# Performance work log

Measured on AMD Instinct MI355X. Metric: run time of the kernel, lower is better.

The kernel has to match this reference:

```python
import jax, jax.numpy as jnp
import numpy as np

T, N, E = 8, 5000, 160000
IN_DIM, HID, H = 64, 128, 8
D = HID // H  # head dim = 16
NC = 2
EPS = 1e-5


def layer_norm(x, g, b):
    mu = jnp.mean(x, axis=-1, keepdims=True)
    var = jnp.mean((x - mu) ** 2, axis=-1, keepdims=True)
    return (x - mu) / jnp.sqrt(var + EPS) * g + b


def setup_inputs() -> dict:
    key = jax.random.key(0)
    ks = jax.random.split(key, 24)
    p = {}
    p["x"] = jax.random.normal(ks[0], (T, N, IN_DIM), dtype=jnp.float32)
    p["edge_index"] = jax.random.randint(ks[1], (T, 2, E), 0, N, dtype=jnp.int32)
    p["noise"] = jax.random.normal(ks[2], (N, HID), dtype=jnp.float32)
    def w(k, shape, fan_in):
        return jax.random.normal(k, shape, dtype=jnp.float32) * (1.0 / np.sqrt(fan_in))
    p["W_proj"] = w(ks[3], (IN_DIM, HID), IN_DIM)
    p["b_proj"] = jnp.zeros((HID,), jnp.float32)
    p["W_gat"] = w(ks[4], (HID, HID), HID)
    p["a_src"] = w(ks[5], (H, D), D)
    p["a_dst"] = w(ks[6], (H, D), D)
    p["b_gat"] = jnp.zeros((HID,), jnp.float32)
    p["g1"] = jnp.ones((HID,), jnp.float32)
    p["be1"] = jnp.zeros((HID,), jnp.float32)
    p["W_qkv"] = w(ks[7], (3 * HID, HID), HID)
    p["b_qkv"] = jnp.zeros((3 * HID,), jnp.float32)
    p["W_o"] = w(ks[8], (HID, HID), HID)
    p["b_o"] = jnp.zeros((HID,), jnp.float32)
    p["g2"] = jnp.ones((HID,), jnp.float32)
    p["be2"] = jnp.zeros((HID,), jnp.float32)
    p["Wc1"] = w(ks[9], (HID, HID), HID)
    p["bc1"] = jnp.zeros((HID,), jnp.float32)
    p["gc"] = jnp.ones((HID,), jnp.float32)
    p["bec"] = jnp.zeros((HID,), jnp.float32)
    p["Wc2"] = w(ks[10], (HID, NC), HID)
    p["bc2"] = jnp.array([0.0, 0.1], jnp.float32)
    return p


def reference(x, edge_index, noise, W_proj, b_proj, W_gat, a_src, a_dst, b_gat,
              g1, be1, W_qkv, b_qkv, W_o, b_o, g2, be2,
              Wc1, bc1, gc, bec, Wc2, bc2):
    # per-timestep projection + ReLU: [T, N, HID]
    h = jax.nn.relu(x @ W_proj + b_proj)

    loop = jnp.arange(N, dtype=edge_index.dtype)

    def gat(h_t, ei):  # h_t: [N, HID], ei: [2, E]
        src = jnp.concatenate([ei[0], loop])  # add self loops
        dst = jnp.concatenate([ei[1], loop])
        xh = (h_t @ W_gat).reshape(N, H, D)          # [N, H, D]
        a_s = jnp.sum(xh * a_src, axis=-1)           # [N, H]
        a_d = jnp.sum(xh * a_dst, axis=-1)           # [N, H]
        e = jax.nn.leaky_relu(a_s[src] + a_d[dst], 0.2)  # [E', H]
        m = jax.ops.segment_max(e, dst, num_segments=N)
        ex = jnp.exp(e - m[dst])
        s = jax.ops.segment_sum(ex, dst, num_segments=N)
        alpha = ex / (s[dst] + 1e-16)                # segment softmax per dst/head
        out = jax.ops.segment_sum(xh[src] * alpha[..., None], dst, num_segments=N)
        return out.reshape(N, HID) + b_gat

    feats = jax.vmap(gat)(h, edge_index)             # [T, N, HID]
    nf = jnp.transpose(feats, (1, 0, 2))             # [N, T, HID] (node = batch)

    nrm = layer_norm(nf, g1, be1)
    qkv = nrm @ W_qkv.T + b_qkv                      # [N, T, 3*HID]
    q, k, v = jnp.split(qkv, 3, axis=-1)
    def heads(t):
        return t.reshape(N, T, H, D).transpose(0, 2, 1, 3)  # [N, H, T, D]
    q, k, v = heads(q), heads(k), heads(v)
    scores = jnp.einsum('nhqd,nhkd->nhqk', q, k) / jnp.sqrt(jnp.float32(D))
    attn = jax.nn.softmax(scores, axis=-1)
    ta = jnp.einsum('nhqk,nhkd->nhqd', attn, v)
    ta = ta.transpose(0, 2, 1, 3).reshape(N, T, HID) @ W_o.T + b_o

    fused = layer_norm(nf + ta, g2, be2)
    emb = fused[:, -1, :]                            # [N, HID]

    node_ids = jnp.arange(N, dtype=jnp.float32) / N
    div = jnp.sin(node_ids * 6.28) * 0.1             # [N]
    emb = emb + div[:, None] + noise * 0.05          # eval noise scale

    h1 = emb @ Wc1 + bc1
    h1 = jax.nn.gelu(layer_norm(h1, gc, bec), approximate=False)
    logits = h1 @ Wc2 + bc2                          # [N, 2]
    sinu = jnp.sin(jnp.arange(N, dtype=jnp.float32) * 0.5) * 0.2
    logits = logits.at[:, 1].add(sinu)
    return emb, logits
```

## Files before the change

### kernel.cpp

```cpp
#include <hip/hip_runtime.h>
#include <math.h>

#define T 8
#define N 5000
#define E 160000
#define EN (E + N)
#define IN_DIM 64
#define HID 128
#define H 8
#define D 16
#define NC 2
#define MT 32
#define NB 4

__device__ __forceinline__ float leaky(float e) { return (e >= 0.0f) ? e : 0.2f * e; }

__global__ __launch_bounds__(256) void k_pg(const float* __restrict__ x,
                                            const float* __restrict__ Wp,
                                            const float* __restrict__ bp,
                                            const float* __restrict__ Wg,
                                            const float* __restrict__ asrc,
                                            const float* __restrict__ adst,
                                            float* __restrict__ xh,
                                            float* __restrict__ a_s,
                                            float* __restrict__ a_d,
                                            int* __restrict__ cursor) {
    __shared__ float xt[MT][IN_DIM];
    __shared__ float ht[MT][HID + 1];
    int row0 = blockIdx.x * MT;
    int tid = threadIdx.x;

    {
        int gi = blockIdx.x * 256 + tid;
        if (gi < T * N) cursor[gi] = 0;
    }

    for (int idx = tid; idx < MT * IN_DIM; idx += 256) {
        int r = idx >> 6, k = idx & 63;
        xt[r][k] = x[(size_t)(row0 + r) * IN_DIM + k];
    }
    __syncthreads();

    int cg = tid & 31;
    int rg = tid >> 5;
    int c0 = cg * 4, r0 = rg * 4;

    {
        float4 b4 = *(const float4*)(bp + c0);
        float a00=b4.x,a01=b4.y,a02=b4.z,a03=b4.w;
        float a10=b4.x,a11=b4.y,a12=b4.z,a13=b4.w;
        float a20=b4.x,a21=b4.y,a22=b4.z,a23=b4.w;
        float a30=b4.x,a31=b4.y,a32=b4.z,a33=b4.w;
        for (int k = 0; k < IN_DIM; ++k) {
            float4 w = *(const float4*)(Wp + (size_t)k * HID + c0);
            float x0 = xt[r0 + 0][k], x1 = xt[r0 + 1][k];
            float x2 = xt[r0 + 2][k], x3 = xt[r0 + 3][k];
            a00 += x0*w.x; a01 += x0*w.y; a02 += x0*w.z; a03 += x0*w.w;
            a10 += x1*w.x; a11 += x1*w.y; a12 += x1*w.z; a13 += x1*w.w;
            a20 += x2*w.x; a21 += x2*w.y; a22 += x2*w.z; a23 += x2*w.w;
            a30 += x3*w.x; a31 += x3*w.y; a32 += x3*w.z; a33 += x3*w.w;
        }
        ht[r0+0][c0+0]=fmaxf(a00,0.f); ht[r0+0][c0+1]=fmaxf(a01,0.f);
        ht[r0+0][c0+2]=fmaxf(a02,0.f); ht[r0+0][c0+3]=fmaxf(a03,0.f);
        ht[r0+1][c0+0]=fmaxf(a10,0.f); ht[r0+1][c0+1]=fmaxf(a11,0.f);
        ht[r0+1][c0+2]=fmaxf(a12,0.f); ht[r0+1][c0+3]=fmaxf(a13,0.f);
        ht[r0+2][c0+0]=fmaxf(a20,0.f); ht[r0+2][c0+1]=fmaxf(a21,0.f);
        ht[r0+2][c0+2]=fmaxf(a22,0.f); ht[r0+2][c0+3]=fmaxf(a23,0.f);
        ht[r0+3][c0+0]=fmaxf(a30,0.f); ht[r0+3][c0+1]=fmaxf(a31,0.f);
        ht[r0+3][c0+2]=fmaxf(a32,0.f); ht[r0+3][c0+3]=fmaxf(a33,0.f);
    }
    __syncthreads();

    float a00=0,a01=0,a02=0,a03=0, a10=0,a11=0,a12=0,a13=0;
    float a20=0,a21=0,a22=0,a23=0, a30=0,a31=0,a32=0,a33=0;
    for (int k = 0; k < HID; ++k) {
        float4 w = *(const float4*)(Wg + (size_t)k * HID + c0);
        float h0 = ht[r0 + 0][k], h1 = ht[r0 + 1][k];
        float h2 = ht[r0 + 2][k], h3 = ht[r0 + 3][k];
        a00 += h0*w.x; a01 += h0*w.y; a02 += h0*w.z; a03 += h0*w.w;
        a10 += h1*w.x; a11 += h1*w.y; a12 += h1*w.z; a13 += h1*w.w;
        a20 += h2*w.x; a21 += h2*w.y; a22 += h2*w.z; a23 += h2*w.w;
        a30 += h3*w.x; a31 += h3*w.y; a32 += h3*w.z; a33 += h3*w.w;
    }
    {
        float4 v;
        v.x=a00; v.y=a01; v.z=a02; v.w=a03;
        *(float4*)(xh + (size_t)(row0 + r0 + 0) * HID + c0) = v;
        v.x=a10; v.y=a11; v.z=a12; v.w=a13;
        *(float4*)(xh + (size_t)(row0 + r0 + 1) * HID + c0) = v;
        v.x=a20; v.y=a21; v.z=a22; v.w=a23;
        *(float4*)(xh + (size_t)(row0 + r0 + 2) * HID + c0) = v;
        v.x=a30; v.y=a31; v.z=a32; v.w=a33;
        *(float4*)(xh + (size_t)(row0 + r0 + 3) * HID + c0) = v;
    }
    __syncthreads();
    ht[r0+0][c0+0]=a00; ht[r0+0][c0+1]=a01; ht[r0+0][c0+2]=a02; ht[r0+0][c0+3]=a03;
    ht[r0+1][c0+0]=a10; ht[r0+1][c0+1]=a11; ht[r0+1][c0+2]=a12; ht[r0+1][c0+3]=a13;
    ht[r0+2][c0+0]=a20; ht[r0+2][c0+1]=a21; ht[r0+2][c0+2]=a22; ht[r0+2][c0+3]=a23;
    ht[r0+3][c0+0]=a30; ht[r0+3][c0+1]=a31; ht[r0+3][c0+2]=a32; ht[r0+3][c0+3]=a33;
    __syncthreads();

    {
        int r = tid >> 3, hh = tid & 7;
        float s1 = 0.0f, s2 = 0.0f;
        #pragma unroll
        for (int d = 0; d < D; ++d) {
            float v = ht[r][hh * D + d];
            s1 += v * asrc[hh * D + d];
            s2 += v * adst[hh * D + d];
        }
        a_s[(size_t)(row0 + r) * H + hh] = s1;
        a_d[(size_t)(row0 + r) * H + hh] = s2;
    }
}

__global__ void k_tr(const float* __restrict__ W_qkv, const float* __restrict__ W_o,
                     float* __restrict__ WTq, float* __restrict__ WoT) {
    int idx = blockIdx.x * 256 + threadIdx.x;
    if (idx < 384 * 128) {
        int j = idx >> 7, c = idx & 127;
        WTq[c * 384 + j] = W_qkv[idx];
    } else if (idx < 384 * 128 + 128 * 128) {
        int r = idx - 384 * 128;
        int j = r >> 7, k = r & 127;
        WoT[k * 128 + j] = W_o[r];
    }
}

__global__ __launch_bounds__(256) void k_hist(const int* __restrict__ ei,
                                              int* __restrict__ cursor) {
    __shared__ int hist[N];
    int t = blockIdx.x >> 3;
    int chunk = blockIdx.x & 7;
    int tid = threadIdx.x;

    for (int i = tid; i < N; i += 256) hist[i] = 0;
    __syncthreads();

    const int CS = (EN + 7) / 8;
    int i0 = chunk * CS;
    int i1 = (i0 + CS < EN) ? i0 + CS : EN;
    const int* drow = ei + (size_t)(2 * t + 1) * E;
    for (int i = i0 + tid; i < i1; i += 256) {
        int d = (i < E) ? drow[i] : (i - E);
        atomicAdd(&hist[d], 1);
    }
    __syncthreads();

    int* cur = cursor + t * N;
    for (int i = tid; i < N; i += 256) {
        int c = hist[i];
        if (c) atomicAdd(&cur[i], c);
    }
}

__global__ void k_scan(int* __restrict__ cursor, int* __restrict__ offs) {
    __shared__ int part[256];
    int t = blockIdx.x;
    int tid = threadIdx.x;
    const int CH = 20;
    int begin = tid * CH;
    int sum = 0;
    for (int k = 0; k < CH; ++k) {
        int i = begin + k;
        if (i < N) sum += cursor[t * N + i];
    }
    part[tid] = sum;
    __syncthreads();
    if (tid == 0) {
        int run = 0;
        for (int i = 0; i < 256; ++i) { int v = part[i]; part[i] = run; run += v; }
        offs[t * (N + 1) + N] = run;
    }
    __syncthreads();
    int run = part[tid];
    for (int k = 0; k < CH; ++k) {
        int i = begin + k;
        if (i < N) {
            int cnt = cursor[t * N + i];
            offs[t * (N + 1) + i] = run;
            cursor[t * N + i] = run;
            run += cnt;
        }
    }
}

__global__ __launch_bounds__(256) void k_scatter(const int* __restrict__ ei,
                                                 int* __restrict__ cursor,
                                                 int* __restrict__ csr_src) {
    const int PT = EN / 4;
    int idx = blockIdx.x * 256 + threadIdx.x;
    int t = idx / PT;
    if (t >= T) return;
    int e0 = idx - t * PT;

    const int* srow = ei + (size_t)(2 * t) * E;
    const int* drow = srow + E;
    int s[4], d[4];
    #pragma unroll
    for (int j = 0; j < 4; ++j) {
        int i = e0 + j * PT;
        if (i < E) { s[j] = srow[i]; d[j] = drow[i]; }
        else       { s[j] = d[j] = i - E; }
    }
    int* cur = cursor + t * N;
    int p[4];
    #pragma unroll
    for (int j = 0; j < 4; ++j) p[j] = atomicAdd(&cur[d[j]], 1);
    int* csb = csr_src + (size_t)t * EN;
    #pragma unroll
    for (int j = 0; j < 4; ++j) csb[p[j]] = s[j];
}

__global__ __launch_bounds__(128) void k_aggc(
        const int* __restrict__ offs, const int* __restrict__ csr_src,
        const float* __restrict__ a_s, const float* __restrict__ a_d,
        const float* __restrict__ xh, const float* __restrict__ b_gat,
        const float* __restrict__ g1, const float* __restrict__ be1,
        float* __restrict__ nrm, float* __restrict__ xlast_g) {
    int b = blockIdx.x;
    int t = b & 7;
    int dst = b >> 3;
    int tid = threadIdx.x;

    int o0 = offs[t * (N + 1) + dst];
    int o1 = offs[t * (N + 1) + dst + 1];
    int deg = o1 - o0;
    const int* esrc = csr_src + (size_t)t * EN + o0;
    const float* as_b = a_s + (size_t)t * N * H;
    const float* ad_b = a_d + (size_t)t * N * H;
    const float* xh_b = xh + (size_t)t * N * HID;

    __shared__ float lal[16][H];
    __shared__ int   lsrc[16];
    __shared__ float ws_s[2][H];
    __shared__ float pacc[2][HID];
    __shared__ float red[128];

    int eh_e = tid >> 3, eh_h = tid & 7;
    int el = tid >> 5, cg = tid & 31;
    int hg = cg >> 2;
    float adh_e = ad_b[dst * H + eh_h];

    float4 acc = {0.0f, 0.0f, 0.0f, 0.0f};
    float wpart = 0.0f;

    int ntile = (deg + 15) >> 4;
    for (int tt = 0; tt < ntile; ++tt) {
        int ej = (tt << 4) + eh_e;
        float w = 0.0f;
        int src = 0;
        if (ej < deg) {
            src = esrc[ej];
            w = expf(leaky(as_b[src * H + eh_h] + adh_e));
        }
        if (eh_h == 0) lsrc[eh_e] = src;
        lal[eh_e][eh_h] = w;
        wpart += w;
        __syncthreads();
        #pragma unroll
        for (int jj = 0; jj < 4; ++jj) {
            int j = (jj << 2) + el;
            int s = lsrc[j];
            float l = lal[j][hg];
            float4 v = *(const float4*)(xh_b + (size_t)s * HID + (cg << 2));
            acc.x += l * v.x; acc.y += l * v.y;
            acc.z += l * v.z; acc.w += l * v.w;
        }
        __syncthreads();
    }

    {
        float w = wpart;
        w += __shfl_xor(w, 8);
        w += __shfl_xor(w, 16);
        w += __shfl_xor(w, 32);
        if ((tid & 63) < 8) ws_s[tid >> 6][eh_h] = w;
    }
    acc.x += __shfl_xor(acc.x, 32);
    acc.y += __shfl_xor(acc.y, 32);
    acc.z += __shfl_xor(acc.z, 32);
    acc.w += __shfl_xor(acc.w, 32);
    if (!(tid & 32)) *(float4*)&pacc[tid >> 6][(tid & 31) << 2] = acc;
    __syncthreads();

    int hh = tid >> 4;
    float wsum = ws_s[0][hh] + ws_s[1][hh];
    float val = (pacc[0][tid] + pacc[1][tid]) / (wsum + 1e-16f);

    float v = val + b_gat[tid];
    red[tid] = v;
    __syncthreads();
    if (tid < 64) {
        float s = red[tid] + red[tid + 64];
        #pragma unroll
        for (int m = 1; m < 64; m <<= 1) s += __shfl_xor(s, m);
        if (tid == 0) red[0] = s;
    }
    __syncthreads();
    float mu = red[0] * (1.0f / HID);
    __syncthreads();
    float dv = v - mu;
    red[tid] = dv * dv;
    __syncthreads();
    if (tid < 64) {
        float s = red[tid] + red[tid + 64];
        #pragma unroll
        for (int m = 1; m < 64; m <<= 1) s += __shfl_xor(s, m);
        if (tid == 0) red[0] = s;
    }
    __syncthreads();
    float rstd = rsqrtf(red[0] * (1.0f / HID) + 1e-5f);

    nrm[(size_t)(dst * T + t) * HID + tid] = dv * rstd * g1[tid] + be1[tid];
    if (t == T - 1) xlast_g[(size_t)dst * HID + tid] = v;
}

__global__ __launch_bounds__(256) void k_fuse(
        const float* __restrict__ nrm,
        const float* __restrict__ WTq,
        const float* __restrict__ b_qkv,
        const float* __restrict__ xlast_g,
        const float* __restrict__ WoT,
        const float* __restrict__ b_o,
        const float* __restrict__ g2, const float* __restrict__ be2,
        const float* __restrict__ noise, float* __restrict__ out) {
    __shared__ float at[NB * T][HID];
    __shared__ float ql[NB][HID];
    __shared__ float ws[8][384];
    float* ta_s = &at[0][0];

    int n0 = blockIdx.x * NB;
    int tid = threadIdx.x;
    int cg = tid & 31, rg = tid >> 5;
    int c0 = cg * 4, r0 = rg * 4;
    int u = rg >> 1;

    {
        const float* srcp = nrm + (size_t)n0 * T * HID;
        for (int idx = tid; idx < NB * T * 32; idx += 256) {
            int r = idx >> 5, c4 = (idx & 31) << 2;
            *(float4*)&at[r][c4] = *(const float4*)(srcp + (size_t)r * HID + c4);
        }
    }

    float ka[4][4], va[4][4], qa[4];
    {
        float4 bk = *(const float4*)(b_qkv + 128 + c0);
        float4 bv = *(const float4*)(b_qkv + 256 + c0);
        #pragma unroll
        for (int i = 0; i < 4; ++i) {
            ka[i][0] = bk.x; ka[i][1] = bk.y; ka[i][2] = bk.z; ka[i][3] = bk.w;
            va[i][0] = bv.x; va[i][1] = bv.y; va[i][2] = bv.z; va[i][3] = bv.w;
        }
        if (rg < 4) {
            float4 bq = *(const float4*)(b_qkv + c0);
            qa[0] = bq.x; qa[1] = bq.y; qa[2] = bq.z; qa[3] = bq.w;
        } else {
            qa[0] = qa[1] = qa[2] = qa[3] = 0.0f;
        }
    }
    __syncthreads();

    const float* atq = at[(rg & 3) * T + (T - 1)];

    for (int kc = 0; kc < 16; ++kc) {
        #pragma unroll
        for (int j = 0; j < 3; ++j) {
            int f = j * 256 + tid;
            int row = f / 96;
            int cc = (f - row * 96) << 2;
            *(float4*)&ws[row][cc] =
                *(const float4*)(WTq + (size_t)(kc * 8 + row) * 384 + cc);
        }
        __syncthreads();

        #pragma unroll
        for (int kk = 0; kk < 8; kk += 4) {
            int k = kc * 8 + kk;
            float4 e0 = *(const float4*)&at[r0 + 0][k];
            float4 e1 = *(const float4*)&at[r0 + 1][k];
            float4 e2 = *(const float4*)&at[r0 + 2][k];
            float4 e3 = *(const float4*)&at[r0 + 3][k];
            float e0a[4] = {e0.x, e0.y, e0.z, e0.w};
            float e1a[4] = {e1.x, e1.y, e1.z, e1.w};
            float e2a[4] = {e2.x, e2.y, e2.z, e2.w};
            float e3a[4] = {e3.x, e3.y, e3.z, e3.w};
            float eqa[4] = {0.f, 0.f, 0.f, 0.f};
            if (rg < 4) {
                float4 eq = *(const float4*)&atq[k];
                eqa[0] = eq.x; eqa[1] = eq.y; eqa[2] = eq.z; eqa[3] = eq.w;
            }
            #pragma unroll
            for (int j = 0; j < 4; ++j) {
                float4 wk = *(const float4*)&ws[kk + j][128 + c0];
                float4 wv = *(const float4*)&ws[kk + j][256 + c0];
                float x0 = e0a[j], x1 = e1a[j], x2 = e2a[j], x3 = e3a[j];
                ka[0][0] += x0*wk.x; ka[0][1] += x0*wk.y; ka[0][2] += x0*wk.z; ka[0][3] += x0*wk.w;
                ka[1][0] += x1*wk.x; ka[1][1] += x1*wk.y; ka[1][2] += x1*wk.z; ka[1][3] += x1*wk.w;
                ka[2][0] += x2*wk.x; ka[2][1] += x2*wk.y; ka[2][2] += x2*wk.z; ka[2][3] += x2*wk.w;
                ka[3][0] += x3*wk.x; ka[3][1] += x3*wk.y; ka[3][2] += x3*wk.z; ka[3][3] += x3*wk.w;
                va[0][0] += x0*wv.x; va[0][1] += x0*wv.y; va[0][2] += x0*wv.z; va[0][3] += x0*wv.w;
                va[1][0] += x1*wv.x; va[1][1] += x1*wv.y; va[1][2] += x1*wv.z; va[1][3] += x1*wv.w;
                va[2][0] += x2*wv.x; va[2][1] += x2*wv.y; va[2][2] += x2*wv.z; va[2][3] += x2*wv.w;
                va[3][0] += x3*wv.x; va[3][1] += x3*wv.y; va[3][2] += x3*wv.z; va[3][3] += x3*wv.w;
                if (rg < 4) {
                    float4 wq = *(const float4*)&ws[kk + j][c0];
                    float xq = eqa[j];
                    qa[0] += xq*wq.x; qa[1] += xq*wq.y; qa[2] += xq*wq.z; qa[3] += xq*wq.w;
                }
            }
        }
        __syncthreads();
    }

    if (rg < 4) {
        float4 q4; q4.x = qa[0]; q4.y = qa[1]; q4.z = qa[2]; q4.w = qa[3];
        *(float4*)&ql[rg][c0] = q4;
    }
    __syncthreads();

    float p0, p1, p2, p3;
    {
        float4 q4 = *(const float4*)&ql[u][c0];
        float ps[4];
        #pragma unroll
        for (int i = 0; i < 4; ++i) {
            float s = q4.x * ka[i][0] + q4.y * ka[i][1]
                    + q4.z * ka[i][2] + q4.w * ka[i][3];
            s += __shfl_xor(s, 1);
            s += __shfl_xor(s, 2);
            ps[i] = s * 0.25f;
        }
        float mx = fmaxf(fmaxf(ps[0], ps[1]), fmaxf(ps[2], ps[3]));
        mx = fmaxf(mx, __shfl_xor(mx, 32));
        float e0 = expf(ps[0] - mx), e1 = expf(ps[1] - mx);
        float e2 = expf(ps[2] - mx), e3 = expf(ps[3] - mx);
        float ssum = e0 + e1 + e2 + e3;
        ssum += __shfl_xor(ssum, 32);
        float inv = 1.0f / ssum;
        p0 = (e0 * va[0][0] + e1 * va[1][0] + e2 * va[2][0] + e3 * va[3][0]) * inv;
        p1 = (e0 * va[0][1] + e1 * va[1][1] + e2 * va[2][1] + e3 * va[3][1]) * inv;
        p2 = (e0 * va[0][2] + e1 * va[1][2] + e2 * va[2][2] + e3 * va[3][2]) * inv;
        p3 = (e0 * va[0][3] + e1 * va[1][3] + e2 * va[2][3] + e3 * va[3][3]) * inv;
        p0 += __shfl_xor(p0, 32);
        p1 += __shfl_xor(p1, 32);
        p2 += __shfl_xor(p2, 32);
        p3 += __shfl_xor(p3, 32);
    }
    if (!(tid & 32)) {
        float4 t4; t4.x = p0; t4.y = p1; t4.z = p2; t4.w = p3;
        *(float4*)&ta_s[u * 128 + c0] = t4;
    }
    __syncthreads();

    {
        int uu = tid >> 6, c = tid & 63;
        int n = n0 + uu;
        float o0 = b_o[c], o1 = b_o[c + 64];
        const float* tar = ta_s + uu * 128;
        #pragma unroll 8
        for (int k = 0; k < HID; k += 4) {
            float t0 = tar[k], t1 = tar[k+1], t2 = tar[k+2], t3 = tar[k+3];
            o0 += t0 * WoT[(size_t)(k+0)*128 + c]  + t1 * WoT[(size_t)(k+1)*128 + c]
                + t2 * WoT[(size_t)(k+2)*128 + c]  + t3 * WoT[(size_t)(k+3)*128 + c];
            o1 += t0 * WoT[(size_t)(k+0)*128 + c+64] + t1 * WoT[(size_t)(k+1)*128 + c+64]
                + t2 * WoT[(size_t)(k+2)*128 + c+64] + t3 * WoT[(size_t)(k+3)*128 + c+64];
        }
        float xa = xlast_g[(size_t)n * HID + c];
        float xb = xlast_g[(size_t)n * HID + c + 64];
        float x2a = xa + o0, x2b = xb + o1;
        float s = x2a + x2b, qs = x2a * x2a + x2b * x2b;
        #pragma unroll
        for (int m = 1; m < 64; m <<= 1) {
            s  += __shfl_xor(s, m);
            qs += __shfl_xor(qs, m);
        }
        float mu = s * (1.0f / HID);
        float var = qs * (1.0f / HID) - mu * mu;
        float rstd = rsqrtf(var + 1e-5f);
        float dv = sinf(((float)n / (float)N) * 6.28f) * 0.1f;
        out[(size_t)n * HID + c] =
            (x2a - mu) * rstd * g2[c] + be2[c] + dv
            + noise[(size_t)n * HID + c] * 0.05f;
        out[(size_t)n * HID + c + 64] =
            (x2b - mu) * rstd * g2[c + 64] + be2[c + 64] + dv
            + noise[(size_t)n * HID + c + 64] * 0.05f;
    }
}

__global__ __launch_bounds__(256) void k_cls(const float* __restrict__ emb,
                                             const float* __restrict__ Wc1,
                                             const float* __restrict__ bc1,
                                             const float* __restrict__ gc,
                                             const float* __restrict__ bec,
                                             const float* __restrict__ Wc2,
                                             const float* __restrict__ bc2,
                                             float* __restrict__ out) {
    __shared__ float et[MT][HID];
    __shared__ float h1t[MT][HID + 1];
    int row0 = blockIdx.x * MT;
    int tid = threadIdx.x;

    for (int idx = tid; idx < MT * HID; idx += 256) {
        int r = idx >> 7, c = idx & 127;
        int row = row0 + r;
        et[r][c] = (row < N) ? emb[(size_t)row * HID + c] : 0.0f;
    }
    __syncthreads();

    {
        int cg = tid & 31, rg = tid >> 5;
        int c0 = cg * 4, r0 = rg * 4;
        float4 b4 = *(const float4*)(bc1 + c0);
        float a00=b4.x,a01=b4.y,a02=b4.z,a03=b4.w;
        float a10=b4.x,a11=b4.y,a12=b4.z,a13=b4.w;
        float a20=b4.x,a21=b4.y,a22=b4.z,a23=b4.w;
        float a30=b4.x,a31=b4.y,a32=b4.z,a33=b4.w;
        for (int k = 0; k < HID; ++k) {
            float4 w = *(const float4*)(Wc1 + (size_t)k * HID + c0);
            float e0 = et[r0 + 0][k], e1 = et[r0 + 1][k];
            float e2 = et[r0 + 2][k], e3 = et[r0 + 3][k];
            a00 += e0*w.x; a01 += e0*w.y; a02 += e0*w.z; a03 += e0*w.w;
            a10 += e1*w.x; a11 += e1*w.y; a12 += e1*w.z; a13 += e1*w.w;
            a20 += e2*w.x; a21 += e2*w.y; a22 += e2*w.z; a23 += e2*w.w;
            a30 += e3*w.x; a31 += e3*w.y; a32 += e3*w.z; a33 += e3*w.w;
        }
        h1t[r0+0][c0+0]=a00; h1t[r0+0][c0+1]=a01; h1t[r0+0][c0+2]=a02; h1t[r0+0][c0+3]=a03;
        h1t[r0+1][c0+0]=a10; h1t[r0+1][c0+1]=a11; h1t[r0+1][c0+2]=a12; h1t[r0+1][c0+3]=a13;
        h1t[r0+2][c0+0]=a20; h1t[r0+2][c0+1]=a21; h1t[r0+2][c0+2]=a22; h1t[r0+2][c0+3]=a23;
        h1t[r0+3][c0+0]=a30; h1t[r0+3][c0+1]=a31; h1t[r0+3][c0+2]=a32; h1t[r0+3][c0+3]=a33;
    }
    __syncthreads();

    {
        int r = tid >> 3, l = tid & 7;
        float p = 0.0f;
        #pragma unroll
        for (int k = 0; k < 16; ++k) p += h1t[r][l + 8 * k];
        #pragma unroll
        for (int m = 1; m < 8; m <<= 1) p += __shfl_xor(p, m);
        float mu = p * (1.0f / HID);
        float v = 0.0f;
        #pragma unroll
        for (int k = 0; k < 16; ++k) { float d = h1t[r][l + 8 * k] - mu; v += d * d; }
        #pragma unroll
        for (int m = 1; m < 8; m <<= 1) v += __shfl_xor(v, m);
        float rstd = rsqrtf(v * (1.0f / HID) + 1e-5f);
        #pragma unroll
        for (int k = 0; k < 16; ++k) {
            int c = l + 8 * k;
            float lnv = (h1t[r][c] - mu) * rstd * gc[c] + bec[c];
            h1t[r][c] = 0.5f * lnv * (1.0f + erff(lnv * 0.70710678118f));
        }
    }
    __syncthreads();

    if (tid < MT * NC) {
        int r = tid >> 1, j = tid & 1;
        int row = row0 + r;
        if (row < N) {
            float acc = bc2[j];
            #pragma unroll 8
            for (int c = 0; c < HID; ++c) acc += h1t[r][c] * Wc2[c * NC + j];
            if (j == 1) acc += sinf((float)row * 0.5f) * 0.2f;
            out[(size_t)N * HID + (size_t)row * NC + j] = acc;
        }
    }
}

extern "C" void kernel_launch(void* const* d_in, const int* in_sizes, int n_in,
                              void* d_out, int out_size, void* d_ws, size_t ws_size,
                              hipStream_t stream) {
    const float* x      = (const float*)d_in[0];
    const int*   ei     = (const int*)d_in[1];
    const float* noise  = (const float*)d_in[2];
    const float* W_proj = (const float*)d_in[3];
    const float* b_proj = (const float*)d_in[4];
    const float* W_gat  = (const float*)d_in[5];
    const float* a_src  = (const float*)d_in[6];
    const float* a_dst  = (const float*)d_in[7];
    const float* b_gat  = (const float*)d_in[8];
    const float* g1     = (const float*)d_in[9];
    const float* be1    = (const float*)d_in[10];
    const float* W_qkv  = (const float*)d_in[11];
    const float* b_qkv  = (const float*)d_in[12];
    const float* W_o    = (const float*)d_in[13];
    const float* b_o    = (const float*)d_in[14];
    const float* g2     = (const float*)d_in[15];
    const float* be2    = (const float*)d_in[16];
    const float* Wc1    = (const float*)d_in[17];
    const float* bc1    = (const float*)d_in[18];
    const float* gc     = (const float*)d_in[19];
    const float* bec    = (const float*)d_in[20];
    const float* Wc2    = (const float*)d_in[21];
    const float* bc2    = (const float*)d_in[22];
    float* out = (float*)d_out;

    float* xh     = (float*)d_ws;
    float* nrm    = xh + 5120000;
    float* a_s    = nrm + 5120000;
    float* a_d    = a_s + 320000;
    int*   offs    = (int*)(a_d + 320000);
    int*   cursor  = offs + 40008;
    int*   csr_src = cursor + 40000;
    float* WTq    = (float*)(csr_src + 1320000);
    float* WoT    = WTq + 49152;
    float* xlastg = WoT + 16384;

    k_tr<<<(384 * 128 + 128 * 128 + 255) / 256, 256, 0, stream>>>(W_qkv, W_o, WTq, WoT);

    k_pg<<<T * N / MT, 256, 0, stream>>>(x, W_proj, b_proj, W_gat, a_src, a_dst,
                                         xh, a_s, a_d, cursor);

    k_hist<<<T * 8, 256, 0, stream>>>(ei, cursor);
    k_scan<<<T, 256, 0, stream>>>(cursor, offs);
    k_scatter<<<(T * (EN / 4) + 255) / 256, 256, 0, stream>>>(ei, cursor, csr_src);

    k_aggc<<<T * N, 128, 0, stream>>>(offs, csr_src, a_s, a_d, xh,
                                      b_gat, g1, be1, nrm, xlastg);

    k_fuse<<<N / NB, 256, 0, stream>>>(nrm, WTq, b_qkv, xlastg, WoT, b_o,
                                       g2, be2, noise, out);

    k_cls<<<(N + MT - 1) / MT, 256, 0, stream>>>(out, Wc1, bc1, gc, bec, Wc2, bc2, out);
}
```

Before: 372.8 us.

## Partition scatter by destination range and register-prefetch QKV weight tiles

The CSR scatter kernel now launches blocks per (timestep, destination range, edge chunk). Each block scans its edge chunk and handles only the edges whose destination falls in its node range, which localizes atomics and csr writes to a smaller region of the cursor and output arrays. In exchange, every edge index is read 8 times. The fuse kernel now prefetches the next weight tile into registers while computing on the current shared tile, overlapping global loads with FMA work.

```diff
diff --git a/kernel.cpp b/kernel.cpp
--- a/kernel.cpp
+++ b/kernel.cpp
@@ -12,6 +12,10 @@
 #define NC 2
 #define MT 32
 #define NB 4
+#define NRR 8
+#define NCHK 32
+#define RSZ ((N + NRR - 1) / NRR)
+#define CSZ ((EN + NCHK - 1) / NCHK)
 
 __device__ __forceinline__ float leaky(float e) { return (e >= 0.0f) ? e : 0.2f * e; }
 
@@ -188,28 +192,30 @@
 __global__ __launch_bounds__(256) void k_scatter(const int* __restrict__ ei,
                                                  int* __restrict__ cursor,
                                                  int* __restrict__ csr_src) {
-    const int PT = EN / 4;
-    int idx = blockIdx.x * 256 + threadIdx.x;
-    int t = idx / PT;
-    if (t >= T) return;
-    int e0 = idx - t * PT;
+    int idx = blockIdx.x;
+    int g = idx & 63;
+    int c = idx >> 6;
+    int t = g >> 3;
+    int r = g & 7;
+    int lo = r * RSZ;
+    int hi = (lo + RSZ < N) ? lo + RSZ : N;
+    int i0 = c * CSZ;
+    int i1 = (i0 + CSZ < EN) ? i0 + CSZ : EN;
 
     const int* srow = ei + (size_t)(2 * t) * E;
     const int* drow = srow + E;
-    int s[4], d[4];
-    #pragma unroll
-    for (int j = 0; j < 4; ++j) {
-        int i = e0 + j * PT;
-        if (i < E) { s[j] = srow[i]; d[j] = drow[i]; }
-        else       { s[j] = d[j] = i - E; }
-    }
     int* cur = cursor + t * N;
-    int p[4];
-    #pragma unroll
-    for (int j = 0; j < 4; ++j) p[j] = atomicAdd(&cur[d[j]], 1);
     int* csb = csr_src + (size_t)t * EN;
-    #pragma unroll
-    for (int j = 0; j < 4; ++j) csb[p[j]] = s[j];
+
+    for (int i = i0 + threadIdx.x; i < i1; i += 256) {
+        int s, d;
+        if (i < E) { d = drow[i]; s = srow[i]; }
+        else       { s = d = i - E; }
+        if (d >= lo && d < hi) {
+            int pos = atomicAdd(&cur[d], 1);
+            csb[pos] = s;
+        }
+    }
 }
 
 __global__ __launch_bounds__(128) void k_aggc(
@@ -360,18 +366,31 @@
             qa[0] = qa[1] = qa[2] = qa[3] = 0.0f;
         }
     }
+
+    int f1 = 256 + tid, f2 = 512 + tid;
+    int sr0 = tid / 96,  sc0 = (tid - sr0 * 96) << 2;
+    int sr1 = f1 / 96,   sc1 = (f1 - sr1 * 96) << 2;
+    int sr2 = f2 / 96,   sc2 = (f2 - sr2 * 96) << 2;
+    const float* wp0 = WTq + (size_t)sr0 * 384 + sc0;
+    const float* wp1 = WTq + (size_t)sr1 * 384 + sc1;
+    const float* wp2 = WTq + (size_t)sr2 * 384 + sc2;
+    float4 wr0 = *(const float4*)wp0;
+    float4 wr1 = *(const float4*)wp1;
+    float4 wr2 = *(const float4*)wp2;
     __syncthreads();
 
     const float* atq = at[(rg & 3) * T + (T - 1)];
 
     for (int kc = 0; kc < 16; ++kc) {
-        #pragma unroll
-        for (int j = 0; j < 3; ++j) {
-            int f = j * 256 + tid;
-            int row = f / 96;
-            int cc = (f - row * 96) << 2;
-            *(float4*)&ws[row][cc] =
-                *(const float4*)(WTq + (size_t)(kc * 8 + row) * 384 + cc);
+        if (kc) __syncthreads();
+        *(float4*)&ws[sr0][sc0] = wr0;
+        *(float4*)&ws[sr1][sc1] = wr1;
+        *(float4*)&ws[sr2][sc2] = wr2;
+        if (kc < 15) {
+            int off = (kc + 1) * 8 * 384;
+            wr0 = *(const float4*)(wp0 + off);
+            wr1 = *(const float4*)(wp1 + off);
+            wr2 = *(const float4*)(wp2 + off);
         }
         __syncthreads();
 
@@ -411,8 +430,8 @@
                 }
             }
         }
-        __syncthreads();
-    }
+    }
+    __syncthreads();
 
     if (rg < 4) {
         float4 q4; q4.x = qa[0]; q4.y = qa[1]; q4.z = qa[2]; q4.w = qa[3];
@@ -615,7 +634,7 @@
 
     k_hist<<<T * 8, 256, 0, stream>>>(ei, cursor);
     k_scan<<<T, 256, 0, stream>>>(cursor, offs);
-    k_scatter<<<(T * (EN / 4) + 255) / 256, 256, 0, stream>>>(ei, cursor, csr_src);
+    k_scatter<<<64 * NCHK, 256, 0, stream>>>(ei, cursor, csr_src);
 
     k_aggc<<<T * N, 128, 0, stream>>>(offs, csr_src, a_s, a_d, xh,
                                       b_gat, g1, be1, nrm, xlastg);
```

New measurement: 372.9 us. About the same (+0.0%).
